# Optimization experiments

Measured on AMD Instinct MI355X. Metric: run time of the kernel, lower is better.

## Reference

```python
import jax, jax.numpy as jnp
import numpy as np

N = 50000      # nodes
E = 800000     # edges (avg degree 16)
D_IN = 64
D_H = 64
D_OUT = 64


def setup_inputs() -> dict:
    key = jax.random.key(0)
    ks = jax.random.split(key, 8)
    x = jax.random.normal(ks[0], (N, D_IN), dtype=jnp.float32)
    edge_index = jax.random.randint(ks[1], (2, E), 0, N, dtype=jnp.int32)
    s1 = 1.0 / np.sqrt(D_IN)
    s2 = 1.0 / np.sqrt(D_H)
    s3 = 1.0 / np.sqrt(D_OUT)
    W1 = jax.random.uniform(ks[2], (D_IN, D_H), jnp.float32, -s1, s1)
    b1 = jnp.zeros((D_H,), jnp.float32)
    W2 = jax.random.uniform(ks[3], (D_H, D_OUT), jnp.float32, -s2, s2)
    b2 = jnp.zeros((D_OUT,), jnp.float32)
    Wfc = jax.random.uniform(ks[4], (D_OUT, 1), jnp.float32, -s3, s3)
    bfc = jax.random.uniform(ks[5], (1,), jnp.float32, -s3, s3)
    return {"x": x, "edge_index": edge_index, "W1": W1, "b1": b1,
            "W2": W2, "b2": b2, "Wfc": Wfc, "bfc": bfc}


def gcn_conv(x, W, b, src, dst, norm, n):
    """PyG GCNConv: h = x@W; out_i = sum_{(s,i)} norm * h_s ; + bias."""
    h = x @ W                                     # [N, d_out]
    msg = h[src] * norm[:, None]                  # [E+N, d_out] gather
    agg = jax.ops.segment_sum(msg, dst, num_segments=n)  # scatter-add
    return agg + b


def reference(x, edge_index, W1, b1, W2, b2, Wfc, bfc):
    n = x.shape[0]
    # add self-loops (PyG default add_self_loops=True)
    loops = jnp.arange(n, dtype=edge_index.dtype)
    src = jnp.concatenate([edge_index[0], loops])
    dst = jnp.concatenate([edge_index[1], loops])
    # symmetric normalization deg^{-1/2} (deg computed with self-loops, >=1)
    deg = jnp.zeros((n,), x.dtype).at[dst].add(1.0)
    dinv = jax.lax.rsqrt(deg)
    norm = dinv[src] * dinv[dst]                  # [E+N]
    h = jax.nn.relu(gcn_conv(x, W1, b1, src, dst, norm, n))
    # dropout is identity in eval mode
    h = jax.nn.relu(gcn_conv(h, W2, b2, src, dst, norm, n))
    out = h @ Wfc + bfc                           # [N, 1]
    out = jnp.mean(out, axis=0, keepdims=True)    # [1, 1]
    return jax.nn.sigmoid(out)
```

## Files before the change

### kernel.cpp

```cpp
#include <hip/hip_runtime.h>
#include <hip/hip_fp16.h>
#include <math.h>

#define N_NODES 50000
#define N_EDGES 800000
#define D_FEAT 64

#define NBUCKET 196
#define PART_BLOCKS 196
#define PART_EPB 4096
#define BCAP 6144

#define GEMM_BLOCKS (N_NODES / 16)
#define AGG_UNITS 1568
#define N_PAD (NBUCKET * 256)

typedef float v2f __attribute__((ext_vector_type(2)));


__device__ __forceinline__ unsigned pack_fp8x4(float a, float b, float c, float d) {
    unsigned w = 0;
    w = __builtin_amdgcn_cvt_pk_fp8_f32(a, b, w, false);
    w = __builtin_amdgcn_cvt_pk_fp8_f32(c, d, w, true);
    return w;
}

__device__ __forceinline__ void addf8(float acc[8], uint2 r) {
    v2f f0 = __builtin_amdgcn_cvt_pk_f32_fp8(r.x, false);
    v2f f1 = __builtin_amdgcn_cvt_pk_f32_fp8(r.x, true);
    v2f f2 = __builtin_amdgcn_cvt_pk_f32_fp8(r.y, false);
    v2f f3 = __builtin_amdgcn_cvt_pk_f32_fp8(r.y, true);
    acc[0] += f0[0]; acc[1] += f0[1];
    acc[2] += f1[0]; acc[3] += f1[1];
    acc[4] += f2[0]; acc[5] += f2[1];
    acc[6] += f3[0]; acc[7] += f3[1];
}


__global__ __launch_bounds__(256) void k_zero(int* __restrict__ gcount) {
    if (threadIdx.x < NBUCKET) gcount[threadIdx.x] = 0;
}

__global__ __launch_bounds__(256) void k_part(const int* __restrict__ src,
                                              const int* __restrict__ dst,
                                              int* __restrict__ gcount,
                                              unsigned* __restrict__ ebuf) {
    __shared__ unsigned eloc[PART_EPB];
    __shared__ int cnt[NBUCKET];
    int tid = threadIdx.x;
    for (int i = tid; i < NBUCKET; i += 256) cnt[i] = 0;
    __syncthreads();
    int e0 = blockIdx.x * PART_EPB;
    int n = N_EDGES - e0; if (n > PART_EPB) n = PART_EPB;
    for (int k = tid; k < n; k += 256) {
        int e = e0 + k;
        int d = dst[e];
        eloc[k] = (unsigned)src[e] | ((unsigned)(d & 255) << 16) | ((unsigned)(d >> 8) << 24);
        atomicAdd(&cnt[d >> 8], 1);
    }
    __syncthreads();
    for (int i = tid; i < NBUCKET; i += 256)
        cnt[i] = atomicAdd(&gcount[i], cnt[i]);
    __syncthreads();
    for (int k = tid; k < n; k += 256) {
        unsigned p = eloc[k];
        int b = p >> 24;
        int slot = atomicAdd(&cnt[b], 1);
        if (slot < BCAP) ebuf[(size_t)b * BCAP + slot] = p;
    }
}

__global__ __launch_bounds__(256) void k_p2group(const unsigned* __restrict__ ebuf,
                                                 const int* __restrict__ gcount,
                                                 int* __restrict__ rowbeg,
                                                 int* __restrict__ rowdeg,
                                                 ushort* __restrict__ colsrc,
                                                 float* __restrict__ dinv) {
    __shared__ unsigned eloc[BCAP];
    __shared__ int hist[256];
    __shared__ int sh[256];
    int tid = threadIdx.x;
    int b = blockIdx.x;
    int cnt = gcount[b]; if (cnt > BCAP) cnt = BCAP;
    hist[tid] = 0;
    __syncthreads();
    for (int i = tid; i < cnt; i += 256) {
        unsigned p = ebuf[(size_t)b * BCAP + i];
        eloc[i] = p;
        atomicAdd(&hist[(p >> 16) & 255], 1);
    }
    __syncthreads();
    int v = hist[tid];
    sh[tid] = v;
    __syncthreads();
    #pragma unroll
    for (int off = 1; off < 256; off <<= 1) {
        int t = (tid >= off) ? sh[tid - off] : 0;
        __syncthreads();
        sh[tid] += t;
        __syncthreads();
    }
    int binoff = sh[tid] - v;
    int node = b * 256 + tid;
    rowbeg[node] = b * BCAP + binoff;
    rowdeg[node] = v;
    dinv[node] = rsqrtf((float)(v + 1));
    hist[tid] = binoff;
    __syncthreads();
    for (int i = tid; i < cnt; i += 256) {
        unsigned p = eloc[i];
        int slot = b * BCAP + atomicAdd(&hist[(p >> 16) & 255], 1);
        colsrc[slot] = (ushort)(p & 0xFFFFu);
    }
}


__global__ __launch_bounds__(256) void k_gemm_f32(const float* __restrict__ X,
                                                  const float* __restrict__ W,
                                                  const float* __restrict__ dinv,
                                                  unsigned* __restrict__ out8) {
    __shared__ float Wl[64][64];
    int tid = threadIdx.x;
    {
        const float4* Wv = (const float4*)W;
        float4* Wlv = (float4*)&Wl[0][0];
        #pragma unroll
        for (int i = 0; i < 4; ++i) Wlv[tid + 256 * i] = Wv[tid + 256 * i];
    }
    __syncthreads();
    int r = blockIdx.x * 16 + (tid >> 4);
    int c0 = (tid & 15) << 2;
    const float4* xrow = (const float4*)(X + (size_t)r * D_FEAT);
    float ax = 0.f, ay = 0.f, az = 0.f, aw = 0.f;
    #pragma unroll
    for (int k4 = 0; k4 < 16; ++k4) {
        float4 xv = xrow[k4];
        #pragma unroll
        for (int j = 0; j < 4; ++j) {
            float xs = (j == 0) ? xv.x : (j == 1) ? xv.y : (j == 2) ? xv.z : xv.w;
            const float4 wv = *(const float4*)&Wl[4 * k4 + j][c0];
            ax += xs * wv.x; ay += xs * wv.y; az += xs * wv.z; aw += xs * wv.w;
        }
    }
    float sc = dinv[r];
    out8[r * 16 + (c0 >> 2)] = pack_fp8x4(ax * sc, ay * sc, az * sc, aw * sc);
}


__device__ __forceinline__ void agg_core(const unsigned char* __restrict__ hm,
                                         const ushort* __restrict__ colsrc,
                                         int beg, int deg, int o, float acc[8]) {
    const uint2* hv = (const uint2*)hm;
    int j = 0;
    for (; j + 8 <= deg; j += 8) {
        int s[8]; uint2 r[8];
        #pragma unroll
        for (int u = 0; u < 8; ++u) s[u] = colsrc[beg + j + u];
        #pragma unroll
        for (int u = 0; u < 8; ++u) r[u] = hv[(size_t)s[u] * 8 + o];
        #pragma unroll
        for (int u = 0; u < 8; ++u) addf8(acc, r[u]);
    }
    if (j + 4 <= deg) {
        int s[4]; uint2 r[4];
        #pragma unroll
        for (int u = 0; u < 4; ++u) s[u] = colsrc[beg + j + u];
        #pragma unroll
        for (int u = 0; u < 4; ++u) r[u] = hv[(size_t)s[u] * 8 + o];
        #pragma unroll
        for (int u = 0; u < 4; ++u) addf8(acc, r[u]);
        j += 4;
    }
    for (; j < deg; ++j) {
        int s = colsrc[beg + j];
        addf8(acc, hv[(size_t)s * 8 + o]);
    }
}


__global__ __launch_bounds__(256) void k_agg1_g2(const unsigned char* __restrict__ hm,
                                                 const int* __restrict__ rowbeg,
                                                 const int* __restrict__ rowdeg,
                                                 const ushort* __restrict__ colsrc,
                                                 const float* __restrict__ dinv,
                                                 const float* __restrict__ b1,
                                                 const float* __restrict__ W2,
                                                 unsigned char* __restrict__ outp) {
    __shared__ float Wl[64][64];
    {
        const float4* Wv = (const float4*)W2;
        float4* Wlv = (float4*)&Wl[0][0];
        #pragma unroll
        for (int i = 0; i < 4; ++i) Wlv[threadIdx.x + 256 * i] = Wv[threadIdx.x + 256 * i];
    }
    __syncthreads();
    int lane = threadIdx.x & 63;
    int wid = threadIdx.x >> 6;
    int node = (blockIdx.x * 4 + wid) * 8 + (lane >> 3);
    int o = lane & 7;
    if (node < N_NODES) {
        float acc[8];
        #pragma unroll
        for (int i = 0; i < 8; ++i) acc[i] = 0.f;
        const uint2* hv = (const uint2*)hm;
        addf8(acc, hv[(size_t)node * 8 + o]);
        agg_core(hm, colsrc, rowbeg[node], rowdeg[node], o, acc);
        float di = dinv[node];
        const float4* b4 = (const float4*)b1;
        float4 bl = b4[o * 2], bh = b4[o * 2 + 1];
        float h1[8];
        h1[0] = fmaxf(di * acc[0] + bl.x, 0.f);
        h1[1] = fmaxf(di * acc[1] + bl.y, 0.f);
        h1[2] = fmaxf(di * acc[2] + bl.z, 0.f);
        h1[3] = fmaxf(di * acc[3] + bl.w, 0.f);
        h1[4] = fmaxf(di * acc[4] + bh.x, 0.f);
        h1[5] = fmaxf(di * acc[5] + bh.y, 0.f);
        h1[6] = fmaxf(di * acc[6] + bh.z, 0.f);
        h1[7] = fmaxf(di * acc[7] + bh.w, 0.f);
        float oa[8];
        #pragma unroll
        for (int i = 0; i < 8; ++i) oa[i] = 0.f;
        int gbase = lane & 56;
        #pragma unroll
        for (int g = 0; g < 8; ++g) {
            #pragma unroll
            for (int j = 0; j < 8; ++j) {
                float hk = __shfl(h1[j], gbase | g, 64);
                const float4 w0 = *(const float4*)&Wl[g * 8 + j][o * 8];
                const float4 w1 = *(const float4*)&Wl[g * 8 + j][o * 8 + 4];
                oa[0] += hk * w0.x; oa[1] += hk * w0.y;
                oa[2] += hk * w0.z; oa[3] += hk * w0.w;
                oa[4] += hk * w1.x; oa[5] += hk * w1.y;
                oa[6] += hk * w1.z; oa[7] += hk * w1.w;
            }
        }
        uint2 st;
        st.x = pack_fp8x4(oa[0] * di, oa[1] * di, oa[2] * di, oa[3] * di);
        st.y = pack_fp8x4(oa[4] * di, oa[5] * di, oa[6] * di, oa[7] * di);
        *(uint2*)(outp + (size_t)node * D_FEAT + o * 8) = st;
    }
}


__global__ __launch_bounds__(256) void k_agg2_dot(const unsigned char* __restrict__ hm,
                                                  const int* __restrict__ rowbeg,
                                                  const int* __restrict__ rowdeg,
                                                  const ushort* __restrict__ colsrc,
                                                  const float* __restrict__ dinv,
                                                  const float* __restrict__ bias,
                                                  const float* __restrict__ Wfc,
                                                  float* __restrict__ partials) {
    __shared__ float red[4];
    int lane = threadIdx.x & 63;
    int wid = threadIdx.x >> 6;
    int node = (blockIdx.x * 4 + wid) * 8 + (lane >> 3);
    int o = lane & 7;
    float s = 0.f;
    if (node < N_NODES) {
        float acc[8];
        #pragma unroll
        for (int i = 0; i < 8; ++i) acc[i] = 0.f;
        const uint2* hv = (const uint2*)hm;
        addf8(acc, hv[(size_t)node * 8 + o]);
        agg_core(hm, colsrc, rowbeg[node], rowdeg[node], o, acc);
        float di = dinv[node];
        const float4* b4 = (const float4*)bias;
        const float4* w4 = (const float4*)Wfc;
        float4 bl = b4[o * 2], bh = b4[o * 2 + 1];
        float4 wl = w4[o * 2], wh = w4[o * 2 + 1];
        s  = fmaxf(di * acc[0] + bl.x, 0.f) * wl.x;
        s += fmaxf(di * acc[1] + bl.y, 0.f) * wl.y;
        s += fmaxf(di * acc[2] + bl.z, 0.f) * wl.z;
        s += fmaxf(di * acc[3] + bl.w, 0.f) * wl.w;
        s += fmaxf(di * acc[4] + bh.x, 0.f) * wh.x;
        s += fmaxf(di * acc[5] + bh.y, 0.f) * wh.y;
        s += fmaxf(di * acc[6] + bh.z, 0.f) * wh.z;
        s += fmaxf(di * acc[7] + bh.w, 0.f) * wh.w;
    }
    #pragma unroll
    for (int m = 1; m < 64; m <<= 1) s += __shfl_xor(s, m, 64);
    if (lane == 0) red[wid] = s;
    __syncthreads();
    if (threadIdx.x == 0) partials[blockIdx.x] = red[0] + red[1] + red[2] + red[3];
}

__global__ __launch_bounds__(256) void k_final(const float* __restrict__ partials,
                                               const float* __restrict__ bfc,
                                               float* __restrict__ out) {
    __shared__ float red[4];
    float s = 0.0f;
    for (int i = threadIdx.x; i < AGG_UNITS; i += 256) s += partials[i];
    #pragma unroll
    for (int off = 32; off > 0; off >>= 1) s += __shfl_down(s, off, 64);
    if ((threadIdx.x & 63) == 0) red[threadIdx.x >> 6] = s;
    __syncthreads();
    if (threadIdx.x == 0) {
        float t = red[0] + red[1] + red[2] + red[3];
        float z = t / (float)N_NODES + bfc[0];
        out[0] = 1.0f / (1.0f + expf(-z));
    }
}


extern "C" void kernel_launch(void* const* d_in, const int* in_sizes, int n_in,
                              void* d_out, int out_size, void* d_ws, size_t ws_size,
                              hipStream_t stream) {
    const float* x   = (const float*)d_in[0];
    const int*   ei  = (const int*)d_in[1];
    const int*   src = ei;
    const int*   dst = ei + N_EDGES;
    const float* W1  = (const float*)d_in[2];
    const float* b1  = (const float*)d_in[3];
    const float* W2  = (const float*)d_in[4];
    const float* b2  = (const float*)d_in[5];
    const float* Wfc = (const float*)d_in[6];
    const float* bfc = (const float*)d_in[7];
    float* out = (float*)d_out;

    char* ws = (char*)d_ws;
    size_t off = 0;
    auto alloc = [&](size_t bytes) -> char* {
        char* p = ws + off;
        off += (bytes + 255) & ~(size_t)255;
        return p;
    };
    int*           gcount   = (int*)alloc((size_t)NBUCKET * 4);
    unsigned*      ebuf     = (unsigned*)alloc((size_t)NBUCKET * BCAP * 4);
    ushort*        colsrc   = (ushort*)alloc((size_t)NBUCKET * BCAP * 2);
    int*           rowbeg   = (int*)alloc((size_t)N_PAD * 4);
    int*           rowdeg   = (int*)alloc((size_t)N_PAD * 4);
    float*         dinv     = (float*)alloc((size_t)N_PAD * 4);
    float*         partials = (float*)alloc((size_t)AGG_UNITS * 4);
    unsigned char* bufA     = (unsigned char*)alloc((size_t)N_NODES * D_FEAT);
    unsigned char* bufB     = (unsigned char*)alloc((size_t)N_NODES * D_FEAT);

    k_zero     <<<1,           256, 0, stream>>>(gcount);
    k_part     <<<PART_BLOCKS, 256, 0, stream>>>(src, dst, gcount, ebuf);
    k_p2group  <<<NBUCKET,     256, 0, stream>>>(ebuf, gcount, rowbeg, rowdeg, colsrc, dinv);

    k_gemm_f32 <<<GEMM_BLOCKS, 256, 0, stream>>>(x, W1, dinv, (unsigned*)bufA);

    k_agg1_g2  <<<AGG_UNITS,   256, 0, stream>>>(bufA, rowbeg, rowdeg, colsrc, dinv, b1, W2, bufB);

    k_agg2_dot <<<AGG_UNITS,   256, 0, stream>>>(bufB, rowbeg, rowdeg, colsrc, dinv, b2, Wfc, partials);

    k_final    <<<1,           256, 0, stream>>>(partials, bfc, out);
}
```

Before: 80.62 us.

## Fuse final reduction into agg2 via last-block atomic and widen partition kernels

Removes the separate k_final launch by having the last-finishing agg2 block, detected through an atomic counter, reduce the partials and write the sigmoid output. k_part now uses 391 blocks of 2048 edges and keeps packed edges in registers instead of shared memory, which raises parallelism. k_p2group runs with 512 threads to speed the bucket fill and scatter. The changes cut one kernel launch and raise occupancy, at the cost of a threadfence and atomic in every agg2 block.

```diff
diff --git a/kernel.cpp b/kernel.cpp
--- a/kernel.cpp
+++ b/kernel.cpp
@@ -7,8 +7,8 @@
 #define D_FEAT 64
 
 #define NBUCKET 196
-#define PART_BLOCKS 196
-#define PART_EPB 4096
+#define PART_BLOCKS 391
+#define PART_EPB 2048
 #define BCAP 6144
 
 #define GEMM_BLOCKS (N_NODES / 16)
@@ -38,39 +38,45 @@
 
 
 __global__ __launch_bounds__(256) void k_zero(int* __restrict__ gcount) {
-    if (threadIdx.x < NBUCKET) gcount[threadIdx.x] = 0;
+    if (threadIdx.x < NBUCKET + 1) gcount[threadIdx.x] = 0;
 }
 
 __global__ __launch_bounds__(256) void k_part(const int* __restrict__ src,
                                               const int* __restrict__ dst,
                                               int* __restrict__ gcount,
                                               unsigned* __restrict__ ebuf) {
-    __shared__ unsigned eloc[PART_EPB];
     __shared__ int cnt[NBUCKET];
     int tid = threadIdx.x;
     for (int i = tid; i < NBUCKET; i += 256) cnt[i] = 0;
     __syncthreads();
     int e0 = blockIdx.x * PART_EPB;
-    int n = N_EDGES - e0; if (n > PART_EPB) n = PART_EPB;
-    for (int k = tid; k < n; k += 256) {
-        int e = e0 + k;
-        int d = dst[e];
-        eloc[k] = (unsigned)src[e] | ((unsigned)(d & 255) << 16) | ((unsigned)(d >> 8) << 24);
-        atomicAdd(&cnt[d >> 8], 1);
+    unsigned pw[8];
+    #pragma unroll
+    for (int u = 0; u < 8; ++u) {
+        int e = e0 + u * 256 + tid;
+        pw[u] = 0xFFFFFFFFu;
+        if (e < N_EDGES) {
+            int d = dst[e];
+            pw[u] = (unsigned)src[e] | ((unsigned)(d & 255) << 16) | ((unsigned)(d >> 8) << 24);
+            atomicAdd(&cnt[d >> 8], 1);
+        }
     }
     __syncthreads();
     for (int i = tid; i < NBUCKET; i += 256)
         cnt[i] = atomicAdd(&gcount[i], cnt[i]);
     __syncthreads();
-    for (int k = tid; k < n; k += 256) {
-        unsigned p = eloc[k];
+    #pragma unroll
+    for (int u = 0; u < 8; ++u) {
+        unsigned p = pw[u];
         int b = p >> 24;
-        int slot = atomicAdd(&cnt[b], 1);
-        if (slot < BCAP) ebuf[(size_t)b * BCAP + slot] = p;
-    }
-}
-
-__global__ __launch_bounds__(256) void k_p2group(const unsigned* __restrict__ ebuf,
+        if (b < NBUCKET) {
+            int slot = atomicAdd(&cnt[b], 1);
+            if (slot < BCAP) ebuf[(size_t)b * BCAP + slot] = p;
+        }
+    }
+}
+
+__global__ __launch_bounds__(512) void k_p2group(const unsigned* __restrict__ ebuf,
                                                  const int* __restrict__ gcount,
                                                  int* __restrict__ rowbeg,
                                                  int* __restrict__ rowdeg,
@@ -82,32 +88,34 @@
     int tid = threadIdx.x;
     int b = blockIdx.x;
     int cnt = gcount[b]; if (cnt > BCAP) cnt = BCAP;
-    hist[tid] = 0;
-    __syncthreads();
-    for (int i = tid; i < cnt; i += 256) {
+    if (tid < 256) hist[tid] = 0;
+    __syncthreads();
+    for (int i = tid; i < cnt; i += 512) {
         unsigned p = ebuf[(size_t)b * BCAP + i];
         eloc[i] = p;
         atomicAdd(&hist[(p >> 16) & 255], 1);
     }
     __syncthreads();
-    int v = hist[tid];
-    sh[tid] = v;
+    int v = (tid < 256) ? hist[tid] : 0;
+    if (tid < 256) sh[tid] = v;
     __syncthreads();
     #pragma unroll
     for (int off = 1; off < 256; off <<= 1) {
-        int t = (tid >= off) ? sh[tid - off] : 0;
+        int t = (tid >= off && tid < 256) ? sh[tid - off] : 0;
         __syncthreads();
-        sh[tid] += t;
+        if (tid < 256) sh[tid] += t;
         __syncthreads();
     }
-    int binoff = sh[tid] - v;
-    int node = b * 256 + tid;
-    rowbeg[node] = b * BCAP + binoff;
-    rowdeg[node] = v;
-    dinv[node] = rsqrtf((float)(v + 1));
-    hist[tid] = binoff;
-    __syncthreads();
-    for (int i = tid; i < cnt; i += 256) {
+    if (tid < 256) {
+        int binoff = sh[tid] - v;
+        int node = b * 256 + tid;
+        rowbeg[node] = b * BCAP + binoff;
+        rowdeg[node] = v;
+        dinv[node] = rsqrtf((float)(v + 1));
+        hist[tid] = binoff;
+    }
+    __syncthreads();
+    for (int i = tid; i < cnt; i += 512) {
         unsigned p = eloc[i];
         int slot = b * BCAP + atomicAdd(&hist[(p >> 16) & 255], 1);
         colsrc[slot] = (ushort)(p & 0xFFFFu);
@@ -242,15 +250,19 @@
 }
 
 
-__global__ __launch_bounds__(256) void k_agg2_dot(const unsigned char* __restrict__ hm,
+__global__ __launch_bounds__(256) void k_agg2_fin(const unsigned char* __restrict__ hm,
                                                   const int* __restrict__ rowbeg,
                                                   const int* __restrict__ rowdeg,
                                                   const ushort* __restrict__ colsrc,
                                                   const float* __restrict__ dinv,
                                                   const float* __restrict__ bias,
                                                   const float* __restrict__ Wfc,
-                                                  float* __restrict__ partials) {
+                                                  float* __restrict__ partials,
+                                                  int* __restrict__ done,
+                                                  const float* __restrict__ bfc,
+                                                  float* __restrict__ out) {
     __shared__ float red[4];
+    __shared__ int amLast;
     int lane = threadIdx.x & 63;
     int wid = threadIdx.x >> 6;
     int node = (blockIdx.x * 4 + wid) * 8 + (lane >> 3);
@@ -281,23 +293,27 @@
     for (int m = 1; m < 64; m <<= 1) s += __shfl_xor(s, m, 64);
     if (lane == 0) red[wid] = s;
     __syncthreads();
-    if (threadIdx.x == 0) partials[blockIdx.x] = red[0] + red[1] + red[2] + red[3];
-}
-
-__global__ __launch_bounds__(256) void k_final(const float* __restrict__ partials,
-                                               const float* __restrict__ bfc,
-                                               float* __restrict__ out) {
-    __shared__ float red[4];
-    float s = 0.0f;
-    for (int i = threadIdx.x; i < AGG_UNITS; i += 256) s += partials[i];
-    #pragma unroll
-    for (int off = 32; off > 0; off >>= 1) s += __shfl_down(s, off, 64);
-    if ((threadIdx.x & 63) == 0) red[threadIdx.x >> 6] = s;
-    __syncthreads();
     if (threadIdx.x == 0) {
-        float t = red[0] + red[1] + red[2] + red[3];
-        float z = t / (float)N_NODES + bfc[0];
-        out[0] = 1.0f / (1.0f + expf(-z));
+        partials[blockIdx.x] = red[0] + red[1] + red[2] + red[3];
+        __threadfence();
+        int t = atomicAdd(done, 1);
+        amLast = (t == AGG_UNITS - 1) ? 1 : 0;
+    }
+    __syncthreads();
+    if (amLast) {
+        __threadfence();
+        const volatile float* vp = partials;
+        float s2 = 0.f;
+        for (int i = threadIdx.x; i < AGG_UNITS; i += 256) s2 += vp[i];
+        #pragma unroll
+        for (int off = 32; off > 0; off >>= 1) s2 += __shfl_down(s2, off, 64);
+        if (lane == 0) red[wid] = s2;
+        __syncthreads();
+        if (threadIdx.x == 0) {
+            float t = red[0] + red[1] + red[2] + red[3];
+            float z = t / (float)N_NODES + bfc[0];
+            out[0] = 1.0f / (1.0f + expf(-z));
+        }
     }
 }
 
@@ -324,7 +340,7 @@
         off += (bytes + 255) & ~(size_t)255;
         return p;
     };
-    int*           gcount   = (int*)alloc((size_t)NBUCKET * 4);
+    int*           gcount   = (int*)alloc((size_t)(NBUCKET + 1) * 4);
     unsigned*      ebuf     = (unsigned*)alloc((size_t)NBUCKET * BCAP * 4);
     ushort*        colsrc   = (ushort*)alloc((size_t)NBUCKET * BCAP * 2);
     int*           rowbeg   = (int*)alloc((size_t)N_PAD * 4);
@@ -333,16 +349,16 @@
     float*         partials = (float*)alloc((size_t)AGG_UNITS * 4);
     unsigned char* bufA     = (unsigned char*)alloc((size_t)N_NODES * D_FEAT);
     unsigned char* bufB     = (unsigned char*)alloc((size_t)N_NODES * D_FEAT);
+    int* done = gcount + NBUCKET;
 
     k_zero     <<<1,           256, 0, stream>>>(gcount);
     k_part     <<<PART_BLOCKS, 256, 0, stream>>>(src, dst, gcount, ebuf);
-    k_p2group  <<<NBUCKET,     256, 0, stream>>>(ebuf, gcount, rowbeg, rowdeg, colsrc, dinv);
+    k_p2group  <<<NBUCKET,     512, 0, stream>>>(ebuf, gcount, rowbeg, rowdeg, colsrc, dinv);
 
     k_gemm_f32 <<<GEMM_BLOCKS, 256, 0, stream>>>(x, W1, dinv, (unsigned*)bufA);
 
     k_agg1_g2  <<<AGG_UNITS,   256, 0, stream>>>(bufA, rowbeg, rowdeg, colsrc, dinv, b1, W2, bufB);
 
-    k_agg2_dot <<<AGG_UNITS,   256, 0, stream>>>(bufB, rowbeg, rowdeg, colsrc, dinv, b2, Wfc, partials);
-
-    k_final    <<<1,           256, 0, stream>>>(partials, bfc, out);
-}
+    k_agg2_fin <<<AGG_UNITS,   256, 0, stream>>>(bufB, rowbeg, rowdeg, colsrc, dinv, b2, Wfc,
+                                                 partials, done, bfc, out);
+}
```

After: 109.3 us. 1.36x slower.
